# Kernel optimization log

Hardware: AMD Instinct MI355X
Metric: run time of the kernel (lower is better)

The kernel has to match this reference:

```python
import math
import jax, jax.numpy as jnp
import numpy as np

B, S, H, N = 2, 2048, 1024, 16
HN = H // N
ALPHA = 32.0


def setup_inputs() -> dict:
    key = jax.random.key(0)
    k1, k2, k3, k4, k5 = jax.random.split(key, 5)
    hidden_states = jax.random.normal(k1, (B, S, H), dtype=jnp.float32)
    # lower-triangular causal mask, broadcastable over batch and heads
    ltor_mask = jnp.tril(jnp.ones((S, S), dtype=jnp.float32))[None, None]
    w_qkv = jax.random.normal(k2, (H, 3 * H), dtype=jnp.float32) * 0.02
    b_qkv = jax.random.normal(k3, (3 * H,), dtype=jnp.float32) * 0.02
    w_dense = jax.random.normal(k4, (H, H), dtype=jnp.float32) * 0.02
    b_dense = jax.random.normal(k5, (H,), dtype=jnp.float32) * 0.02
    return {"hidden_states": hidden_states, "ltor_mask": ltor_mask,
            "w_qkv": w_qkv, "b_qkv": b_qkv, "w_dense": w_dense, "b_dense": b_dense}


def reference(hidden_states, ltor_mask, w_qkv, b_qkv, w_dense, b_dense):
    b, s, h = hidden_states.shape
    # fused QKV projection, split into q/k/v chunks along last dim
    qkv = hidden_states @ w_qkv + b_qkv            # [b, s, 3h]
    q, k, v = jnp.split(qkv, 3, axis=-1)
    # [b, s, h] -> [b, n, s, hn]
    def heads(t):
        return t.reshape(b, s, N, HN).transpose(0, 2, 1, 3)
    q, k, v = heads(q), heads(k), heads(v)
    # pb-relax: scale q before the matmul
    scores = jnp.einsum('bnqd,bnkd->bnqk', q / math.sqrt(HN), k)  # [b, n, s, s]
    mask = ltor_mask[:, :, -s:]                    # [1, 1, s, s]
    scores = scores * mask - 10000.0 * (1.0 - mask)
    # pb-relax max-subtraction stabilization (max over both score dims per head)
    ss = scores / ALPHA
    m = jax.lax.stop_gradient(jnp.max(ss.reshape(b, N, -1), axis=-1))[:, :, None, None]
    scores = (ss - m) * ALPHA
    probs = jax.nn.softmax(scores, axis=-1)        # dropout prob = 0
    ctx = jnp.einsum('bnqk,bnkd->bnqd', probs, v)  # [b, n, s, hn]
    ctx = ctx.transpose(0, 2, 1, 3).reshape(b, s, h)
    out = ctx @ w_dense + b_dense
    return out
```

## Files before the change

kernel.cpp:

```cpp
#include <hip/hip_runtime.h>
#include <hip/hip_bf16.h>
#include <stdint.h>

#define BB 2
#define SS 2048
#define HH 1024

typedef unsigned short u16;
typedef uint32_t u32;
typedef short bf8v __attribute__((ext_vector_type(8)));
typedef float f4 __attribute__((ext_vector_type(4)));

#define QSCALE 0.18033688011112042f

__device__ __forceinline__ u16 f2bf(float f) {
    u32 u = __builtin_bit_cast(u32, f);
    u = (u + 0x7fffu + ((u >> 16) & 1u)) >> 16;
    return (u16)u;
}

__device__ __forceinline__ u16 bfbits(float f) {
    return __builtin_bit_cast(u16, __float2bfloat16(f));
}

__device__ __forceinline__ void async16(const void* g, void* lds) {
    __builtin_amdgcn_global_load_lds(
        (const __attribute__((address_space(1))) u32*)g,
        (__attribute__((address_space(3))) u32*)lds, 16, 0, 0);
}

__global__ void cast_f32_bf16(const float* __restrict__ in, u16* __restrict__ out, int n) {
    int i = (blockIdx.x * blockDim.x + threadIdx.x) * 4;
    if (i < n) {
        float4 v = *(const float4*)(in + i);
        ushort4 o;
        o.x = f2bf(v.x); o.y = f2bf(v.y); o.z = f2bf(v.z); o.w = f2bf(v.w);
        *(ushort4*)(out + i) = o;
    }
}

__global__ void transpose_cast(const float* __restrict__ w, u16* __restrict__ wt, int K, int Nn) {
    __shared__ float tile[32][33];
    int tn = blockIdx.x, tk = blockIdx.y;
    int c = threadIdx.x & 31, r0 = threadIdx.x >> 5;
#pragma unroll
    for (int it = 0; it < 4; ++it) {
        int r = r0 + it * 8;
        tile[r][c] = w[(size_t)(tk * 32 + r) * Nn + tn * 32 + c];
    }
    __syncthreads();
#pragma unroll
    for (int it = 0; it < 4; ++it) {
        int r = r0 + it * 8;
        wt[(size_t)(tn * 32 + r) * K + tk * 32 + c] = f2bf(tile[c][r]);
    }
}

template<int EPI>
__global__ __launch_bounds__(256) void gemm_bt(
    const u16* __restrict__ A, const u16* __restrict__ Bt,
    const float* __restrict__ bias, void* __restrict__ Cout,
    int M, int N, int K)
{
    __shared__ __align__(16) u16 As[128 * 64];
    __shared__ __align__(16) u16 Bs[128 * 64];
    const int m0 = blockIdx.y * 128, n0 = blockIdx.x * 128;
    const int t = threadIdx.x, w = t >> 6, l = t & 63;
    const int wr = w >> 1, wc = w & 1;

    f4 acc[4][4];
#pragma unroll
    for (int i = 0; i < 4; ++i)
#pragma unroll
        for (int j = 0; j < 4; ++j) acc[i][j] = (f4){0.f, 0.f, 0.f, 0.f};

    const int nk = K >> 6;
    for (int kt = 0; kt < nk; ++kt) {
        const int k0 = kt << 6;
#pragma unroll
        for (int i = 0; i < 4; ++i) {
            int chunk = w * 256 + i * 64 + l;
            int row = chunk >> 3, seg = chunk & 7;
            int segg = seg ^ (row & 7);
            async16(A + (size_t)(m0 + row) * K + k0 + segg * 8,
                    (char*)As + (w * 256 + i * 64) * 16);
        }
#pragma unroll
        for (int i = 0; i < 4; ++i) {
            int chunk = w * 256 + i * 64 + l;
            int row = chunk >> 3, seg = chunk & 7;
            int segg = seg ^ (row & 7);
            async16(Bt + (size_t)(n0 + row) * K + k0 + segg * 8,
                    (char*)Bs + (w * 256 + i * 64) * 16);
        }
        __syncthreads();
#pragma unroll
        for (int kk = 0; kk < 2; ++kk) {
            bf8v af[4], bq[4];
#pragma unroll
            for (int fq = 0; fq < 4; ++fq) {
                int row = wr * 64 + fq * 16 + (l & 15);
                af[fq] = *(const bf8v*)((const char*)As +
                    ((row * 128 + kk * 64 + ((l >> 4) * 16)) ^ ((row & 7) << 4)));
            }
#pragma unroll
            for (int fr = 0; fr < 4; ++fr) {
                int row = wc * 64 + fr * 16 + (l & 15);
                bq[fr] = *(const bf8v*)((const char*)Bs +
                    ((row * 128 + kk * 64 + ((l >> 4) * 16)) ^ ((row & 7) << 4)));
            }
#pragma unroll
            for (int fq = 0; fq < 4; ++fq)
#pragma unroll
                for (int fr = 0; fr < 4; ++fr)
                    acc[fq][fr] = __builtin_amdgcn_mfma_f32_16x16x32_bf16(
                        af[fq], bq[fr], acc[fq][fr], 0, 0, 0);
        }
        __syncthreads();
    }
#pragma unroll
    for (int fq = 0; fq < 4; ++fq) {
#pragma unroll
        for (int fr = 0; fr < 4; ++fr) {
            int col = n0 + wc * 64 + fr * 16 + (l & 15);
            float bv = bias[col];
#pragma unroll
            for (int j = 0; j < 4; ++j) {
                int row = m0 + wr * 64 + fq * 16 + ((l >> 4) * 4) + j;
                float v = acc[fq][fr][j] + bv;
                if (EPI == 0) {
                    if (col < HH) v *= QSCALE;
                    ((u16*)Cout)[(size_t)row * N + col] = f2bf(v);
                } else {
                    ((float*)Cout)[(size_t)row * N + col] = v;
                }
            }
        }
    }
}

__global__ __launch_bounds__(256, 4) void attn_kernel(
    const u16* __restrict__ qkv,
    u16* __restrict__ ctx,
    float* __restrict__ pO,
    float* __restrict__ pL)
{
    __shared__ __align__(16) char sm[40960];

    const int bid = blockIdx.x;
    const int head = (bid & 7) * 4 + (bid >> 8);
    const int p    = (bid >> 3) & 15;
    const int h    = (bid >> 7) & 1;
    const int b = head >> 4, n = head & 15;
    const int w = threadIdx.x >> 6, l = threadIdx.x & 63;
    const int q16 = l & 15, hi = l >> 4;
    const size_t rs = 3072;

    const int qtA = p, qtB = 31 - p;
    const int ntA = p + 1;
    const int slot = head * 16 + (qtB - 16);
    const int s0 = h ? 17 : 0, s1 = h ? 33 : 17;

    const u16* kb0   = qkv + (size_t)(b * SS) * rs + HH + n * 64;
    const u16* vbase = qkv + (size_t)(b * SS) * rs + 2 * HH + n * 64;

    const int m_   = (q16 & 7) << 4;
    const int krd0 = (q16 * 128 + hi * 16) ^ m_;
    const int krd1 = (q16 * 128 + 64 + hi * 16) ^ m_;
    const int psw  = 32768 + w * 2048;
    const int par0 = psw + krd0, par1 = psw + krd1;
    const int pstb = psw + q16 * 128;
    const int pst0 = pstb + ((0  + hi * 8) ^ m_);
    const int pst1 = pstb + ((32 + hi * 8) ^ m_);
    const int pst2 = pstb + ((64 + hi * 8) ^ m_);
    const int pst3 = pstb + ((96 + hi * 8) ^ m_);
    const int vwb  = 16384 + w * 2048 + (l >> 5) * 1024;
    const int vwl  = (l & 31) * 4;
    const int vrow2 = (l & 31) * 2, vcol = w * 16 + (l >> 5) * 8;

    auto tl = [&](int gs) { return gs < ntA ? gs : gs - ntA; };

    auto stageK = [&](int kt, int buf) {
#pragma unroll
        for (int i = 0; i < 2; ++i) {
            int cbase = w * 128 + i * 64;
            int chunk = cbase + l;
            int row = chunk >> 3, seg = chunk & 7;
            int segg = seg ^ (row & 7);
            async16(kb0 + (size_t)(kt * 64 + row) * rs + segg * 8,
                    sm + buf * 8192 + cbase * 16);
        }
    };
    auto loadV = [&](int kt, bf8v& v0, bf8v& v1) {
        const u16* vp = vbase + (size_t)(kt * 64 + vrow2) * rs + vcol;
        v0 = *(const bf8v*)vp;
        v1 = *(const bf8v*)(vp + rs);
    };
    auto writeVt = [&](int buf, bf8v v0, bf8v v1) {
        char* base = sm + vwb + buf * 8192;
#pragma unroll
        for (int j = 0; j < 8; ++j) {
            u32 pk = (u32)(u16)v0[j] | ((u32)(u16)v1[j] << 16);
            *(u32*)(base + j * 128 + (vwl ^ (j << 4))) = pk;
        }
    };

    bf8v qB0, qB1, cq0, cq1;
    {
        const u16* qq = qkv + (size_t)(b * SS + qtB * 64 + w * 16 + q16) * rs + n * 64;
        qB0 = *(const bf8v*)(qq + hi * 8);
        qB1 = *(const bf8v*)(qq + 32 + hi * 8);
    }
    if (h == 0) {
        const u16* qp = qkv + (size_t)(b * SS + qtA * 64 + w * 16 + q16) * rs + n * 64;
        cq0 = *(const bf8v*)(qp + hi * 8);
        cq1 = *(const bf8v*)(qp + 32 + hi * 8);
    } else { cq0 = qB0; cq1 = qB1; }

    {
        stageK(tl(s0), s0 & 1);
        bf8v v0c, v1c;
        loadV(tl(s0), v0c, v1c);
        writeVt(s0 & 1, v0c, v1c);
    }
    __syncthreads();

    f4 o[4];
#pragma unroll
    for (int od = 0; od < 4; ++od) o[od] = (f4){0.f, 0.f, 0.f, 0.f};
    float lsum = 0.f;

    for (int s = s0; s < s1; ++s) {
        if (h == 0 && s == ntA) {
            u16* cb = ctx + (size_t)(b * SS + qtA * 64 + w * 16) * HH + n * 64;
#pragma unroll
            for (int j = 0; j < 4; ++j) {
                int qrow = hi * 4 + j;
                float inv = 1.0f / __shfl(lsum, qrow);
#pragma unroll
                for (int od = 0; od < 4; ++od)
                    cb[(size_t)qrow * HH + od * 16 + q16] = f2bf(o[od][j] * inv);
            }
#pragma unroll
            for (int od = 0; od < 4; ++od) o[od] = (f4){0.f, 0.f, 0.f, 0.f};
            lsum = 0.f;
            cq0 = qB0; cq1 = qB1;
        }

        const int cur = s & 1, nx = cur ^ 1;
        const bool pf = (s + 1 < s1);
        bf8v nv0, nv1;
        if (pf) { stageK(tl(s + 1), nx); loadV(tl(s + 1), nv0, nv1); }

        const int ka0 = krd0 + (cur << 13);
        const int ka1 = krd1 + (cur << 13);

        f4 sf[4];
#pragma unroll
        for (int fr = 0; fr < 4; ++fr) sf[fr] = (f4){0.f, 0.f, 0.f, 0.f};
        __builtin_amdgcn_s_setprio(1);
#pragma unroll
        for (int fr = 0; fr < 4; ++fr) {
            bf8v kf0 = *(const bf8v*)(sm + ka0 + fr * 2048);
            bf8v kf1 = *(const bf8v*)(sm + ka1 + fr * 2048);
            sf[fr] = __builtin_amdgcn_mfma_f32_16x16x32_bf16(kf0, cq0, sf[fr], 0, 0, 0);
            sf[fr] = __builtin_amdgcn_mfma_f32_16x16x32_bf16(kf1, cq1, sf[fr], 0, 0, 0);
        }
        __builtin_amdgcn_s_setprio(0);

        float pv[4][4];
#pragma unroll
        for (int fr = 0; fr < 4; ++fr)
#pragma unroll
            for (int j = 0; j < 4; ++j) pv[fr][j] = exp2f(sf[fr][j]);
        if ((h == 0 && s == ntA - 1) || s == 32) {
            const int qloc = w * 16 + q16;
#pragma unroll
            for (int fr = 0; fr < 4; ++fr)
#pragma unroll
                for (int j = 0; j < 4; ++j)
                    if (fr * 16 + hi * 4 + j > qloc) pv[fr][j] = 0.f;
        }
        float rsumL = 0.f;
#pragma unroll
        for (int fr = 0; fr < 4; ++fr)
#pragma unroll
            for (int j = 0; j < 4; ++j) rsumL += pv[fr][j];
        rsumL += __shfl_xor(rsumL, 16);
        rsumL += __shfl_xor(rsumL, 32);
        lsum += rsumL;

        {
            u32 a0 = (u32)bfbits(pv[0][0]) | ((u32)bfbits(pv[0][1]) << 16);
            u32 a1 = (u32)bfbits(pv[0][2]) | ((u32)bfbits(pv[0][3]) << 16);
            *(uint2*)(sm + pst0) = make_uint2(a0, a1);
            u32 b0 = (u32)bfbits(pv[1][0]) | ((u32)bfbits(pv[1][1]) << 16);
            u32 b1 = (u32)bfbits(pv[1][2]) | ((u32)bfbits(pv[1][3]) << 16);
            *(uint2*)(sm + pst1) = make_uint2(b0, b1);
            u32 c0 = (u32)bfbits(pv[2][0]) | ((u32)bfbits(pv[2][1]) << 16);
            u32 c1 = (u32)bfbits(pv[2][2]) | ((u32)bfbits(pv[2][3]) << 16);
            *(uint2*)(sm + pst2) = make_uint2(c0, c1);
            u32 d0 = (u32)bfbits(pv[3][0]) | ((u32)bfbits(pv[3][1]) << 16);
            u32 d1 = (u32)bfbits(pv[3][2]) | ((u32)bfbits(pv[3][3]) << 16);
            *(uint2*)(sm + pst3) = make_uint2(d0, d1);
        }

        __builtin_amdgcn_s_setprio(1);
#pragma unroll
        for (int kk = 0; kk < 2; ++kk) {
            bf8v pa = *(const bf8v*)(sm + (kk ? par1 : par0));
            const int vb_ = 16384 + (cur << 13) + (kk ? krd1 : krd0);
#pragma unroll
            for (int od = 0; od < 4; ++od) {
                bf8v vf = *(const bf8v*)(sm + vb_ + od * 2048);
                o[od] = __builtin_amdgcn_mfma_f32_16x16x32_bf16(pa, vf, o[od], 0, 0, 0);
            }
        }
        __builtin_amdgcn_s_setprio(0);

        if (pf) writeVt(nx, nv0, nv1);
        __syncthreads();
    }

    float* po = pO + (size_t)slot * 4096;
#pragma unroll
    for (int j = 0; j < 4; ++j) {
        int qrow = w * 16 + hi * 4 + j;
#pragma unroll
        for (int od = 0; od < 4; ++od)
            atomicAdd(po + qrow * 64 + od * 16 + q16, o[od][j]);
    }
    if (hi == 0) atomicAdd(pL + slot * 64 + w * 16 + q16, lsum);
}

__global__ __launch_bounds__(256) void norm_kernel(
    const float* __restrict__ pO, const float* __restrict__ pL,
    u16* __restrict__ ctx)
{
    const int slot = blockIdx.x;
    const int head = slot >> 4;
    const int qt = 16 + (slot & 15);
    const int b = head >> 4, n = head & 15;
    const float* po = pO + (size_t)slot * 4096;
#pragma unroll
    for (int i = 0; i < 16; ++i) {
        int e = threadIdx.x + 256 * i;
        int row = e >> 6, col = e & 63;
        float v = po[e];
        float lv = pL[slot * 64 + row];
        ctx[(size_t)(b * SS + qt * 64 + row) * HH + n * 64 + col] = f2bf(v / lv);
    }
}

extern "C" void kernel_launch(void* const* d_in, const int* in_sizes, int n_in,
                              void* d_out, int out_size, void* d_ws, size_t ws_size,
                              hipStream_t stream)
{
    const float* hidden  = (const float*)d_in[0];
    const float* w_qkv   = (const float*)d_in[2];
    const float* b_qkv   = (const float*)d_in[3];
    const float* w_dense = (const float*)d_in[4];
    const float* b_dense = (const float*)d_in[5];

    u16* wdT    = (u16*)d_ws;
    u16* ctx_bf = wdT + (size_t)1024 * 1024;
    u16* qkv_bf = ctx_bf + (size_t)4096 * 1024;
    u16* hid_bf = qkv_bf + (size_t)4096 * 3072;
    u16* wqkvT  = hid_bf + (size_t)4096 * 1024;
    float* pO   = (float*)hid_bf;
    float* pL   = pO + (size_t)512 * 4096;

    cast_f32_bf16<<<4096, 256, 0, stream>>>(hidden, hid_bf, 4096 * 1024);
    transpose_cast<<<dim3(96, 32), 256, 0, stream>>>(w_qkv, wqkvT, 1024, 3072);
    transpose_cast<<<dim3(32, 32), 256, 0, stream>>>(w_dense, wdT, 1024, 1024);

    gemm_bt<0><<<dim3(24, 32), 256, 0, stream>>>(hid_bf, wqkvT, b_qkv, qkv_bf,
                                                 4096, 3072, 1024);
    hipMemsetAsync(pO, 0, (size_t)(512 * 4096 + 512 * 64) * 4, stream);
    attn_kernel<<<1024, 256, 0, stream>>>(qkv_bf, ctx_bf, pO, pL);
    norm_kernel<<<512, 256, 0, stream>>>(pO, pL, ctx_bf);
    gemm_bt<1><<<dim3(8, 32), 256, 0, stream>>>(ctx_bf, wdT, b_dense, d_out,
                                                4096, 1024, 1024);
}
```

Baseline: 215.7 us.

## Drop split-KV attention partials and fuse prep kernels into one launch

Each attention block now handles a full paired query-tile pass of 33 KV steps itself, instead of splitting the work in half across two blocks that combined results with atomics, a memset and a separate normalize kernel. The block count halves and the launch bound drops to 2 waves per SIMD. The three input-preparation kernels (hidden cast and two weight transposes) are merged into one launch, and the workspace layout is reshuffled so ctx reuses the hidden buffer. This removes the memset, the atomics and two launches, but loses parallelism, since only 512 longer blocks now fill the GPU.

```diff
diff --git a/kernel.cpp b/kernel.cpp
--- a/kernel.cpp
+++ b/kernel.cpp
@@ -29,19 +29,10 @@
         (__attribute__((address_space(3))) u32*)lds, 16, 0, 0);
 }
 
-__global__ void cast_f32_bf16(const float* __restrict__ in, u16* __restrict__ out, int n) {
-    int i = (blockIdx.x * blockDim.x + threadIdx.x) * 4;
-    if (i < n) {
-        float4 v = *(const float4*)(in + i);
-        ushort4 o;
-        o.x = f2bf(v.x); o.y = f2bf(v.y); o.z = f2bf(v.z); o.w = f2bf(v.w);
-        *(ushort4*)(out + i) = o;
-    }
-}
-
-__global__ void transpose_cast(const float* __restrict__ w, u16* __restrict__ wt, int K, int Nn) {
-    __shared__ float tile[32][33];
-    int tn = blockIdx.x, tk = blockIdx.y;
+__device__ __forceinline__ void transpose_tile(
+    const float* __restrict__ w, u16* __restrict__ wt, int K, int Nn,
+    int tn, int tk, float (*tile)[33])
+{
     int c = threadIdx.x & 31, r0 = threadIdx.x >> 5;
 #pragma unroll
     for (int it = 0; it < 4; ++it) {
@@ -53,6 +44,28 @@
     for (int it = 0; it < 4; ++it) {
         int r = r0 + it * 8;
         wt[(size_t)(tn * 32 + r) * K + tk * 32 + c] = f2bf(tile[c][r]);
+    }
+}
+
+__global__ __launch_bounds__(256) void prep_fused(
+    const float* __restrict__ hidden, const float* __restrict__ w_qkv,
+    const float* __restrict__ w_dense,
+    u16* __restrict__ hid_bf, u16* __restrict__ wqkvT, u16* __restrict__ wdT)
+{
+    __shared__ float tile[32][33];
+    const int bid = blockIdx.x;
+    if (bid < 4096) {
+        int i = (bid * 256 + threadIdx.x) * 4;
+        float4 v = *(const float4*)(hidden + i);
+        ushort4 o;
+        o.x = f2bf(v.x); o.y = f2bf(v.y); o.z = f2bf(v.z); o.w = f2bf(v.w);
+        *(ushort4*)(hid_bf + i) = o;
+    } else if (bid < 7168) {
+        int t = bid - 4096;
+        transpose_tile(w_qkv, wqkvT, 1024, 3072, t % 96, t / 96, tile);
+    } else {
+        int t = bid - 7168;
+        transpose_tile(w_dense, wdT, 1024, 1024, t % 32, t / 32, tile);
     }
 }
 
@@ -139,18 +152,15 @@
     }
 }
 
-__global__ __launch_bounds__(256, 4) void attn_kernel(
+__global__ __launch_bounds__(256, 2) void attn_kernel(
     const u16* __restrict__ qkv,
-    u16* __restrict__ ctx,
-    float* __restrict__ pO,
-    float* __restrict__ pL)
+    u16* __restrict__ ctx)
 {
     __shared__ __align__(16) char sm[40960];
 
     const int bid = blockIdx.x;
-    const int head = (bid & 7) * 4 + (bid >> 8);
+    const int head = (bid & 7) * 4 + (bid >> 7);
     const int p    = (bid >> 3) & 15;
-    const int h    = (bid >> 7) & 1;
     const int b = head >> 4, n = head & 15;
     const int w = threadIdx.x >> 6, l = threadIdx.x & 63;
     const int q16 = l & 15, hi = l >> 4;
@@ -158,8 +168,6 @@
 
     const int qtA = p, qtB = 31 - p;
     const int ntA = p + 1;
-    const int slot = head * 16 + (qtB - 16);
-    const int s0 = h ? 17 : 0, s1 = h ? 33 : 17;
 
     const u16* kb0   = qkv + (size_t)(b * SS) * rs + HH + n * 64;
     const u16* vbase = qkv + (size_t)(b * SS) * rs + 2 * HH + n * 64;
@@ -210,18 +218,16 @@
         const u16* qq = qkv + (size_t)(b * SS + qtB * 64 + w * 16 + q16) * rs + n * 64;
         qB0 = *(const bf8v*)(qq + hi * 8);
         qB1 = *(const bf8v*)(qq + 32 + hi * 8);
-    }
-    if (h == 0) {
         const u16* qp = qkv + (size_t)(b * SS + qtA * 64 + w * 16 + q16) * rs + n * 64;
         cq0 = *(const bf8v*)(qp + hi * 8);
         cq1 = *(const bf8v*)(qp + 32 + hi * 8);
-    } else { cq0 = qB0; cq1 = qB1; }
+    }
 
     {
-        stageK(tl(s0), s0 & 1);
+        stageK(0, 0);
         bf8v v0c, v1c;
-        loadV(tl(s0), v0c, v1c);
-        writeVt(s0 & 1, v0c, v1c);
+        loadV(0, v0c, v1c);
+        writeVt(0, v0c, v1c);
     }
     __syncthreads();
 
@@ -230,8 +236,8 @@
     for (int od = 0; od < 4; ++od) o[od] = (f4){0.f, 0.f, 0.f, 0.f};
     float lsum = 0.f;
 
-    for (int s = s0; s < s1; ++s) {
-        if (h == 0 && s == ntA) {
+    for (int s = 0; s < 33; ++s) {
+        if (s == ntA) {
             u16* cb = ctx + (size_t)(b * SS + qtA * 64 + w * 16) * HH + n * 64;
 #pragma unroll
             for (int j = 0; j < 4; ++j) {
@@ -248,7 +254,7 @@
         }
 
         const int cur = s & 1, nx = cur ^ 1;
-        const bool pf = (s + 1 < s1);
+        const bool pf = (s + 1 < 33);
         bf8v nv0, nv1;
         if (pf) { stageK(tl(s + 1), nx); loadV(tl(s + 1), nv0, nv1); }
 
@@ -273,7 +279,7 @@
         for (int fr = 0; fr < 4; ++fr)
 #pragma unroll
             for (int j = 0; j < 4; ++j) pv[fr][j] = exp2f(sf[fr][j]);
-        if ((h == 0 && s == ntA - 1) || s == 32) {
+        if (s == ntA - 1 || s == 32) {
             const int qloc = w * 16 + q16;
 #pragma unroll
             for (int fr = 0; fr < 4; ++fr)
@@ -322,33 +328,14 @@
         __syncthreads();
     }
 
-    float* po = pO + (size_t)slot * 4096;
+    u16* cb = ctx + (size_t)(b * SS + qtB * 64 + w * 16) * HH + n * 64;
 #pragma unroll
     for (int j = 0; j < 4; ++j) {
-        int qrow = w * 16 + hi * 4 + j;
+        int qrow = hi * 4 + j;
+        float inv = 1.0f / __shfl(lsum, qrow);
 #pragma unroll
         for (int od = 0; od < 4; ++od)
-            atomicAdd(po + qrow * 64 + od * 16 + q16, o[od][j]);
-    }
-    if (hi == 0) atomicAdd(pL + slot * 64 + w * 16 + q16, lsum);
-}
-
-__global__ __launch_bounds__(256) void norm_kernel(
-    const float* __restrict__ pO, const float* __restrict__ pL,
-    u16* __restrict__ ctx)
-{
-    const int slot = blockIdx.x;
-    const int head = slot >> 4;
-    const int qt = 16 + (slot & 15);
-    const int b = head >> 4, n = head & 15;
-    const float* po = pO + (size_t)slot * 4096;
-#pragma unroll
-    for (int i = 0; i < 16; ++i) {
-        int e = threadIdx.x + 256 * i;
-        int row = e >> 6, col = e & 63;
-        float v = po[e];
-        float lv = pL[slot * 64 + row];
-        ctx[(size_t)(b * SS + qt * 64 + row) * HH + n * 64 + col] = f2bf(v / lv);
+            cb[(size_t)qrow * HH + od * 16 + q16] = f2bf(o[od][j] * inv);
     }
 }
 
@@ -362,23 +349,17 @@
     const float* w_dense = (const float*)d_in[4];
     const float* b_dense = (const float*)d_in[5];
 
-    u16* wdT    = (u16*)d_ws;
-    u16* ctx_bf = wdT + (size_t)1024 * 1024;
-    u16* qkv_bf = ctx_bf + (size_t)4096 * 1024;
-    u16* hid_bf = qkv_bf + (size_t)4096 * 3072;
+    u16* hid_bf = (u16*)d_ws;
     u16* wqkvT  = hid_bf + (size_t)4096 * 1024;
-    float* pO   = (float*)hid_bf;
-    float* pL   = pO + (size_t)512 * 4096;
-
-    cast_f32_bf16<<<4096, 256, 0, stream>>>(hidden, hid_bf, 4096 * 1024);
-    transpose_cast<<<dim3(96, 32), 256, 0, stream>>>(w_qkv, wqkvT, 1024, 3072);
-    transpose_cast<<<dim3(32, 32), 256, 0, stream>>>(w_dense, wdT, 1024, 1024);
-
+    u16* wdT    = wqkvT  + (size_t)3072 * 1024;
+    u16* qkv_bf = wdT    + (size_t)1024 * 1024;
+    u16* ctx_bf = hid_bf;
+
+    prep_fused<<<8192, 256, 0, stream>>>(hidden, w_qkv, w_dense,
+                                         hid_bf, wqkvT, wdT);
     gemm_bt<0><<<dim3(24, 32), 256, 0, stream>>>(hid_bf, wqkvT, b_qkv, qkv_bf,
                                                  4096, 3072, 1024);
-    hipMemsetAsync(pO, 0, (size_t)(512 * 4096 + 512 * 64) * 4, stream);
-    attn_kernel<<<1024, 256, 0, stream>>>(qkv_bf, ctx_bf, pO, pL);
-    norm_kernel<<<512, 256, 0, stream>>>(pO, pL, ctx_bf);
+    attn_kernel<<<512, 256, 0, stream>>>(qkv_bf, ctx_bf);
     gemm_bt<1><<<dim3(8, 32), 256, 0, stream>>>(ctx_bf, wdT, b_dense, d_out,
                                                 4096, 1024, 1024);
 }
```

New measurement: 212.7 us. About the same (-1.4%).
